# Kernel optimization log

Measured on AMD Instinct MI355X. Metric: run time of the kernel, lower is better.

Reference implementation:

```python
import jax, jax.numpy as jnp
import numpy as np

EPSILON = 0.0

def setup_inputs() -> dict:
    key = jax.random.key(0)
    k1, k2, k3, k4, k5 = jax.random.split(key, 5)
    N, MAX_NB, D_IN, D_OUT, N_BONDS = 50000, 16, 256, 256, 400000
    x = jax.random.normal(k1, (N, D_IN), dtype=jnp.float32)
    W = jax.random.normal(k2, (D_OUT, D_IN), dtype=jnp.float32) * (1.0 / np.sqrt(D_IN))
    b = jax.random.normal(k3, (D_OUT,), dtype=jnp.float32) * 0.01
    b_from_a = jax.random.randint(k4, (N_BONDS,), 0, N, dtype=jnp.int32)
    a_from_b = jax.random.randint(k5, (N, MAX_NB), 0, N_BONDS, dtype=jnp.int32)
    return {"x": x, "W": W, "b": b, "b_from_a": b_from_a, "a_from_b": a_from_b}

def reference(x, W, b, b_from_a, a_from_b):
    # a2a[i, k] = source atom of the k-th neighbor bond of atom i
    a2a = b_from_a[a_from_b]                      # [N, max_nb]
    h = x @ W.T + b                               # [N, d_out]
    h = h.at[0].set(0.0)                          # row 0 is padding
    message = h[a2a]                              # [N, max_nb, d_out] gather
    out = (1.0 + EPSILON) * h + jnp.sum(message, axis=1)
    return jax.nn.relu(out)
```

## Files before the change

### kernel.cpp

```cpp
#include <hip/hip_runtime.h>

typedef short bf16x8 __attribute__((ext_vector_type(8)));
typedef float f32x4  __attribute__((ext_vector_type(4)));

__device__ __forceinline__ unsigned short f32_to_bf16(float f) {
  union { float f; unsigned int u; } v; v.f = f;
  unsigned int u = v.u;
  u += 0x7fffu + ((u >> 16) & 1u);
  return (unsigned short)(u >> 16);
}
__device__ __forceinline__ float bf16lo_to_f32(unsigned int u) {
  union { unsigned int u; float f; } v; v.u = u << 16; return v.f;
}
__device__ __forceinline__ float bf16hi_to_f32(unsigned int u) {
  union { unsigned int u; float f; } v; v.u = u & 0xffff0000u; return v.f;
}

#define LDSTRIDE 40

__global__ __launch_bounds__(256, 2) void gin_gemm(
    const float* __restrict__ x, const float* __restrict__ W,
    const float* __restrict__ bias, unsigned short* __restrict__ h, int M) {
  __shared__ __align__(16) unsigned short Xs[64 * LDSTRIDE];
  __shared__ __align__(16) unsigned short Ws[256 * LDSTRIDE];

  const int tid  = threadIdx.x;
  const int wid  = tid >> 6;
  const int lane = tid & 63;
  const int row0 = blockIdx.x * 64;

  f32x4 acc[4][4] = {};

  const int srow = tid >> 2;
  const int sk0  = (tid & 3) << 3;
  int agrow = row0 + srow;
  if (agrow >= M) agrow = M - 1;
  const float* aRow = x + (size_t)agrow * 256 + sk0;
  const float* bRow = W + (size_t)srow * 256 + sk0;

  const int quad = lane >> 4;
  const int c16  = lane & 15;
  float4 biasv[4];
#pragma unroll
  for (int ng = 0; ng < 4; ++ng)
    biasv[ng] = *(const float4*)(bias + wid * 64 + ng * 16 + quad * 4);

  for (int kt = 0; kt < 8; ++kt) {
    const int kb = kt * 32;
    {
      float4 v0 = *(const float4*)(aRow + kb);
      float4 v1 = *(const float4*)(aRow + kb + 4);
      bf16x8 u;
      u[0] = (short)f32_to_bf16(v0.x); u[1] = (short)f32_to_bf16(v0.y);
      u[2] = (short)f32_to_bf16(v0.z); u[3] = (short)f32_to_bf16(v0.w);
      u[4] = (short)f32_to_bf16(v1.x); u[5] = (short)f32_to_bf16(v1.y);
      u[6] = (short)f32_to_bf16(v1.z); u[7] = (short)f32_to_bf16(v1.w);
      *(bf16x8*)(&Xs[srow * LDSTRIDE + sk0]) = u;
    }
#pragma unroll
    for (int j = 0; j < 4; ++j) {
      const float* p = bRow + (size_t)(j * 64) * 256 + kb;
      float4 v0 = *(const float4*)p;
      float4 v1 = *(const float4*)(p + 4);
      bf16x8 u;
      u[0] = (short)f32_to_bf16(v0.x); u[1] = (short)f32_to_bf16(v0.y);
      u[2] = (short)f32_to_bf16(v0.z); u[3] = (short)f32_to_bf16(v0.w);
      u[4] = (short)f32_to_bf16(v1.x); u[5] = (short)f32_to_bf16(v1.y);
      u[6] = (short)f32_to_bf16(v1.z); u[7] = (short)f32_to_bf16(v1.w);
      *(bf16x8*)(&Ws[(j * 64 + srow) * LDSTRIDE + sk0]) = u;
    }
    __syncthreads();

    const int r16 = lane & 15;
    const int qk  = (lane >> 4) << 3;
    bf16x8 wf[4], xf[4];
#pragma unroll
    for (int g = 0; g < 4; ++g)
      wf[g] = *(const bf16x8*)(&Ws[(wid * 64 + g * 16 + r16) * LDSTRIDE + qk]);
#pragma unroll
    for (int g = 0; g < 4; ++g)
      xf[g] = *(const bf16x8*)(&Xs[(g * 16 + r16) * LDSTRIDE + qk]);
#pragma unroll
    for (int ng = 0; ng < 4; ++ng)
#pragma unroll
      for (int ag = 0; ag < 4; ++ag)
        acc[ng][ag] = __builtin_amdgcn_mfma_f32_16x16x32_bf16(
            wf[ng], xf[ag], acc[ng][ag], 0, 0, 0);
    __syncthreads();
  }

#pragma unroll
  for (int ag = 0; ag < 4; ++ag) {
    const int atom = row0 + ag * 16 + c16;
    if (atom >= M) continue;
#pragma unroll
    for (int ng = 0; ng < 4; ++ng) {
      const int n0 = wid * 64 + ng * 16 + quad * 4;
      float v0 = acc[ng][ag][0] + biasv[ng].x;
      float v1 = acc[ng][ag][1] + biasv[ng].y;
      float v2 = acc[ng][ag][2] + biasv[ng].z;
      float v3 = acc[ng][ag][3] + biasv[ng].w;
      if (atom == 0) { v0 = v1 = v2 = v3 = 0.0f; }
      uint2 pk;
      pk.x = (unsigned int)f32_to_bf16(v0) | ((unsigned int)f32_to_bf16(v1) << 16);
      pk.y = (unsigned int)f32_to_bf16(v2) | ((unsigned int)f32_to_bf16(v3) << 16);
      *(uint2*)(h + (size_t)atom * 256 + n0) = pk;
    }
  }
}

__global__ __launch_bounds__(256, 4) void gin_gather(
    const unsigned short* __restrict__ h, const int* __restrict__ b_from_a,
    const int* __restrict__ a_from_b, float* __restrict__ out, int N) {
  const int wid  = threadIdx.x >> 6;
  const int lane = threadIdx.x & 63;
  const int i = blockIdx.x * 4 + wid;
  if (i >= N) return;

  const int half = lane >> 5;
  const int hl   = lane & 31;
  const int c0   = hl << 3;

  int src = 0;
  if (lane < 16) src = b_from_a[a_from_b[i * 16 + lane]];

  const unsigned short* hp = h + c0;

  float a0, a1, a2, a3, a4, a5, a6, a7;
  {
    uint4 v = *(const uint4*)(hp + (size_t)i * 256);
    const float selfw = half ? 0.0f : 1.0f;
    a0 = selfw * bf16lo_to_f32(v.x); a1 = selfw * bf16hi_to_f32(v.x);
    a2 = selfw * bf16lo_to_f32(v.y); a3 = selfw * bf16hi_to_f32(v.y);
    a4 = selfw * bf16lo_to_f32(v.z); a5 = selfw * bf16hi_to_f32(v.z);
    a6 = selfw * bf16lo_to_f32(v.w); a7 = selfw * bf16hi_to_f32(v.w);
  }
#pragma unroll
  for (int k = 0; k < 8; ++k) {
    int s = __shfl(src, half * 8 + k, 64);
    uint4 v = *(const uint4*)(hp + (size_t)s * 256);
    a0 += bf16lo_to_f32(v.x); a1 += bf16hi_to_f32(v.x);
    a2 += bf16lo_to_f32(v.y); a3 += bf16hi_to_f32(v.y);
    a4 += bf16lo_to_f32(v.z); a5 += bf16hi_to_f32(v.z);
    a6 += bf16lo_to_f32(v.w); a7 += bf16hi_to_f32(v.w);
  }
  a0 += __shfl_xor(a0, 32, 64); a1 += __shfl_xor(a1, 32, 64);
  a2 += __shfl_xor(a2, 32, 64); a3 += __shfl_xor(a3, 32, 64);
  a4 += __shfl_xor(a4, 32, 64); a5 += __shfl_xor(a5, 32, 64);
  a6 += __shfl_xor(a6, 32, 64); a7 += __shfl_xor(a7, 32, 64);

  float4 r;
  if (half == 0) {
    r.x = fmaxf(a0, 0.0f); r.y = fmaxf(a1, 0.0f);
    r.z = fmaxf(a2, 0.0f); r.w = fmaxf(a3, 0.0f);
  } else {
    r.x = fmaxf(a4, 0.0f); r.y = fmaxf(a5, 0.0f);
    r.z = fmaxf(a6, 0.0f); r.w = fmaxf(a7, 0.0f);
  }
  *(float4*)(out + (size_t)i * 256 + c0 + half * 4) = r;
}

extern "C" void kernel_launch(void* const* d_in, const int* in_sizes, int n_in,
                              void* d_out, int out_size, void* d_ws, size_t ws_size,
                              hipStream_t stream) {
  const float* x        = (const float*)d_in[0];
  const float* W        = (const float*)d_in[1];
  const float* b        = (const float*)d_in[2];
  const int*   b_from_a = (const int*)d_in[3];
  const int*   a_from_b = (const int*)d_in[4];
  float*       out      = (float*)d_out;
  const int M = in_sizes[0] / 256;

  unsigned short* h = (unsigned short*)d_ws;

  gin_gemm<<<(M + 63) / 64, 256, 0, stream>>>(x, W, b, h, M);
  gin_gather<<<(M + 3) / 4, 256, 0, stream>>>(h, b_from_a, a_from_b, out, M);
}
```

Before: 194.9 us.

## Retile GEMM to 128x128 blocks over a 2D grid and batch gather loads

The GEMM now tiles 128 rows by 128 output columns on a 2D grid instead of 64 rows by all 256 columns. This changes how much of W each block converts and stages in shared memory, and reshapes each wave's MFMA tile from 4x4 to 2x8. The gather kernel now issues all eight neighbour-row loads before accumulating, which exposes more memory-level parallelism. The trade-off is that each x row is read and converted twice, once per column half, and more registers are live in the gather.

```diff
diff --git a/kernel.cpp b/kernel.cpp
--- a/kernel.cpp
+++ b/kernel.cpp
@@ -21,81 +21,86 @@
 __global__ __launch_bounds__(256, 2) void gin_gemm(
     const float* __restrict__ x, const float* __restrict__ W,
     const float* __restrict__ bias, unsigned short* __restrict__ h, int M) {
-  __shared__ __align__(16) unsigned short Xs[64 * LDSTRIDE];
-  __shared__ __align__(16) unsigned short Ws[256 * LDSTRIDE];
+  __shared__ __align__(16) unsigned short Xs[128 * LDSTRIDE];
+  __shared__ __align__(16) unsigned short Ws[128 * LDSTRIDE];
 
   const int tid  = threadIdx.x;
   const int wid  = tid >> 6;
   const int lane = tid & 63;
-  const int row0 = blockIdx.x * 64;
+  const int row0  = blockIdx.x * 128;
+  const int ncol0 = blockIdx.y * 128;
 
-  f32x4 acc[4][4] = {};
+  f32x4 acc[2][8] = {};
 
   const int srow = tid >> 2;
   const int sk0  = (tid & 3) << 3;
-  int agrow = row0 + srow;
-  if (agrow >= M) agrow = M - 1;
-  const float* aRow = x + (size_t)agrow * 256 + sk0;
-  const float* bRow = W + (size_t)srow * 256 + sk0;
+  int ar0 = row0 + srow;        if (ar0 >= M) ar0 = M - 1;
+  int ar1 = row0 + 64 + srow;   if (ar1 >= M) ar1 = M - 1;
+  const float* aRow0 = x + (size_t)ar0 * 256 + sk0;
+  const float* aRow1 = x + (size_t)ar1 * 256 + sk0;
+  const float* bRow0 = W + (size_t)(ncol0 + srow) * 256 + sk0;
+  const float* bRow1 = W + (size_t)(ncol0 + 64 + srow) * 256 + sk0;
 
   const int quad = lane >> 4;
   const int c16  = lane & 15;
-  float4 biasv[4];
+  float4 biasv[2];
 #pragma unroll
-  for (int ng = 0; ng < 4; ++ng)
-    biasv[ng] = *(const float4*)(bias + wid * 64 + ng * 16 + quad * 4);
+  for (int ng = 0; ng < 2; ++ng)
+    biasv[ng] = *(const float4*)(bias + ncol0 + wid * 32 + ng * 16 + quad * 4);
 
   for (int kt = 0; kt < 8; ++kt) {
     const int kb = kt * 32;
-    {
-      float4 v0 = *(const float4*)(aRow + kb);
-      float4 v1 = *(const float4*)(aRow + kb + 4);
+#pragma unroll
+    for (int p = 0; p < 2; ++p) {
+      const float* src = p ? aRow1 : aRow0;
+      float4 v0 = *(const float4*)(src + kb);
+      float4 v1 = *(const float4*)(src + kb + 4);
       bf16x8 u;
       u[0] = (short)f32_to_bf16(v0.x); u[1] = (short)f32_to_bf16(v0.y);
       u[2] = (short)f32_to_bf16(v0.z); u[3] = (short)f32_to_bf16(v0.w);
       u[4] = (short)f32_to_bf16(v1.x); u[5] = (short)f32_to_bf16(v1.y);
       u[6] = (short)f32_to_bf16(v1.z); u[7] = (short)f32_to_bf16(v1.w);
-      *(bf16x8*)(&Xs[srow * LDSTRIDE + sk0]) = u;
+      *(bf16x8*)(&Xs[(p * 64 + srow) * LDSTRIDE + sk0]) = u;
     }
 #pragma unroll
-    for (int j = 0; j < 4; ++j) {
-      const float* p = bRow + (size_t)(j * 64) * 256 + kb;
-      float4 v0 = *(const float4*)p;
-      float4 v1 = *(const float4*)(p + 4);
+    for (int p = 0; p < 2; ++p) {
+      const float* src = p ? bRow1 : bRow0;
+      float4 v0 = *(const float4*)(src + kb);
+      float4 v1 = *(const float4*)(src + kb + 4);
       bf16x8 u;
       u[0] = (short)f32_to_bf16(v0.x); u[1] = (short)f32_to_bf16(v0.y);
       u[2] = (short)f32_to_bf16(v0.z); u[3] = (short)f32_to_bf16(v0.w);
       u[4] = (short)f32_to_bf16(v1.x); u[5] = (short)f32_to_bf16(v1.y);
       u[6] = (short)f32_to_bf16(v1.z); u[7] = (short)f32_to_bf16(v1.w);
-      *(bf16x8*)(&Ws[(j * 64 + srow) * LDSTRIDE + sk0]) = u;
+      *(bf16x8*)(&Ws[(p * 64 + srow) * LDSTRIDE + sk0]) = u;
     }
     __syncthreads();
 
     const int r16 = lane & 15;
     const int qk  = (lane >> 4) << 3;
-    bf16x8 wf[4], xf[4];
+    bf16x8 wf[2], xf[8];
 #pragma unroll
-    for (int g = 0; g < 4; ++g)
-      wf[g] = *(const bf16x8*)(&Ws[(wid * 64 + g * 16 + r16) * LDSTRIDE + qk]);
+    for (int g = 0; g < 2; ++g)
+      wf[g] = *(const bf16x8*)(&Ws[(wid * 32 + g * 16 + r16) * LDSTRIDE + qk]);
 #pragma unroll
-    for (int g = 0; g < 4; ++g)
+    for (int g = 0; g < 8; ++g)
       xf[g] = *(const bf16x8*)(&Xs[(g * 16 + r16) * LDSTRIDE + qk]);
 #pragma unroll
-    for (int ng = 0; ng < 4; ++ng)
+    for (int ng = 0; ng < 2; ++ng)
 #pragma unroll
-      for (int ag = 0; ag < 4; ++ag)
+      for (int ag = 0; ag < 8; ++ag)
         acc[ng][ag] = __builtin_amdgcn_mfma_f32_16x16x32_bf16(
             wf[ng], xf[ag], acc[ng][ag], 0, 0, 0);
     __syncthreads();
   }
 
 #pragma unroll
-  for (int ag = 0; ag < 4; ++ag) {
+  for (int ag = 0; ag < 8; ++ag) {
     const int atom = row0 + ag * 16 + c16;
     if (atom >= M) continue;
 #pragma unroll
-    for (int ng = 0; ng < 4; ++ng) {
-      const int n0 = wid * 64 + ng * 16 + quad * 4;
+    for (int ng = 0; ng < 2; ++ng) {
+      const int n0 = ncol0 + wid * 32 + ng * 16 + quad * 4;
       float v0 = acc[ng][ag][0] + biasv[ng].x;
       float v1 = acc[ng][ag][1] + biasv[ng].y;
       float v2 = acc[ng][ag][2] + biasv[ng].z;
@@ -126,23 +131,27 @@
 
   const unsigned short* hp = h + c0;
 
-  float a0, a1, a2, a3, a4, a5, a6, a7;
-  {
-    uint4 v = *(const uint4*)(hp + (size_t)i * 256);
-    const float selfw = half ? 0.0f : 1.0f;
-    a0 = selfw * bf16lo_to_f32(v.x); a1 = selfw * bf16hi_to_f32(v.x);
-    a2 = selfw * bf16lo_to_f32(v.y); a3 = selfw * bf16hi_to_f32(v.y);
-    a4 = selfw * bf16lo_to_f32(v.z); a5 = selfw * bf16hi_to_f32(v.z);
-    a6 = selfw * bf16lo_to_f32(v.w); a7 = selfw * bf16hi_to_f32(v.w);
-  }
+  int s[8];
+#pragma unroll
+  for (int k = 0; k < 8; ++k) s[k] = __shfl(src, half * 8 + k, 64);
+
+  uint4 vself = *(const uint4*)(hp + (size_t)i * 256);
+  uint4 v[8];
+#pragma unroll
+  for (int k = 0; k < 8; ++k)
+    v[k] = *(const uint4*)(hp + (size_t)s[k] * 256);
+
+  const float selfw = half ? 0.0f : 1.0f;
+  float a0 = selfw * bf16lo_to_f32(vself.x), a1 = selfw * bf16hi_to_f32(vself.x);
+  float a2 = selfw * bf16lo_to_f32(vself.y), a3 = selfw * bf16hi_to_f32(vself.y);
+  float a4 = selfw * bf16lo_to_f32(vself.z), a5 = selfw * bf16hi_to_f32(vself.z);
+  float a6 = selfw * bf16lo_to_f32(vself.w), a7 = selfw * bf16hi_to_f32(vself.w);
 #pragma unroll
   for (int k = 0; k < 8; ++k) {
-    int s = __shfl(src, half * 8 + k, 64);
-    uint4 v = *(const uint4*)(hp + (size_t)s * 256);
-    a0 += bf16lo_to_f32(v.x); a1 += bf16hi_to_f32(v.x);
-    a2 += bf16lo_to_f32(v.y); a3 += bf16hi_to_f32(v.y);
-    a4 += bf16lo_to_f32(v.z); a5 += bf16hi_to_f32(v.z);
-    a6 += bf16lo_to_f32(v.w); a7 += bf16hi_to_f32(v.w);
+    a0 += bf16lo_to_f32(v[k].x); a1 += bf16hi_to_f32(v[k].x);
+    a2 += bf16lo_to_f32(v[k].y); a3 += bf16hi_to_f32(v[k].y);
+    a4 += bf16lo_to_f32(v[k].z); a5 += bf16hi_to_f32(v[k].z);
+    a6 += bf16lo_to_f32(v[k].w); a7 += bf16hi_to_f32(v[k].w);
   }
   a0 += __shfl_xor(a0, 32, 64); a1 += __shfl_xor(a1, 32, 64);
   a2 += __shfl_xor(a2, 32, 64); a3 += __shfl_xor(a3, 32, 64);
@@ -173,6 +182,7 @@
 
   unsigned short* h = (unsigned short*)d_ws;
 
-  gin_gemm<<<(M + 63) / 64, 256, 0, stream>>>(x, W, b, h, M);
+  dim3 ggrid((M + 127) / 128, 2);
+  gin_gemm<<<ggrid, 256, 0, stream>>>(x, W, b, h, M);
   gin_gather<<<(M + 3) / 4, 256, 0, stream>>>(h, b_from_a, a_from_b, out, M);
 }
```

Result: slower. 202.1 us (+3.7%).
